# Kernel tuning notes

Hardware: AMD Instinct MI355X
Metric: run time of the kernel (lower is better)

Reference implementation:

```python
import jax, jax.numpy as jnp
import numpy as np

VOCAB, ENC, DEC, ATT, EMB = 10000, 2048, 512, 512, 512
B, P, L = 64, 196, 20


def setup_inputs() -> dict:
    key = jax.random.key(0)
    ks = jax.random.split(key, 24)
    s = lambda k, shape, fan: jax.random.normal(k, shape, jnp.float32) / np.sqrt(fan)
    inp = {
        "img_features": jax.random.normal(ks[0], (B, P, ENC), jnp.float32),
        "captions": jax.random.randint(ks[1], (B, L), 0, VOCAB),
        # init-state projections
        "W_init_h": s(ks[2], (DEC, ENC), ENC), "b_init_h": jnp.zeros((DEC,), jnp.float32),
        "W_init_c": s(ks[3], (DEC, ENC), ENC), "b_init_c": jnp.zeros((DEC,), jnp.float32),
        # attention
        "W_dec": s(ks[4], (ATT, DEC), DEC), "b_dec": jnp.zeros((ATT,), jnp.float32),
        "W_enc": s(ks[5], (ATT, ENC), ENC), "b_enc": jnp.zeros((ATT,), jnp.float32),
        "W_fin": s(ks[6], (1, ATT), ATT), "b_fin": jnp.zeros((1,), jnp.float32),
        # gate + output + embedding
        "W_gate": s(ks[7], (ENC, DEC), DEC), "b_gate": jnp.zeros((ENC,), jnp.float32),
        "W_out": s(ks[8], (VOCAB, DEC), DEC), "b_out": jnp.zeros((VOCAB,), jnp.float32),
        "emb": s(ks[9], (VOCAB, EMB), EMB),
        # LSTMCell (PyTorch gate order: i, f, g, o)
        "W_ih": s(ks[10], (4 * DEC, EMB + ENC), EMB + ENC), "b_ih": jnp.zeros((4 * DEC,), jnp.float32),
        "W_hh": s(ks[11], (4 * DEC, DEC), DEC), "b_hh": jnp.zeros((4 * DEC,), jnp.float32),
    }
    return inp


def _decode(img_features, captions, W_init_h, b_init_h, W_init_c, b_init_c,
            W_dec, b_dec, W_enc, b_enc, W_fin, b_fin,
            W_gate, b_gate, W_out, b_out, emb, W_ih, W_hh, b_ih, b_hh):
    # lengths are uniform (padded tensor), so sort/restore are identity and
    # batch_size_t == B at every step.
    avg = img_features.mean(axis=1)                              # [B,ENC]
    h0 = jnp.tanh(avg @ W_init_h.T + b_init_h)                   # [B,DEC]
    c0 = jnp.tanh(avg @ W_init_c.T + b_init_c)
    enc_proj = img_features @ W_enc.T + b_enc                    # [B,P,ATT] (loop-invariant)
    emb_seq = emb[captions[:, :-1]]                              # [B,T,EMB], T = L-1

    def step(carry, e_t):
        h, c = carry
        U_h = h @ W_dec.T + b_dec                                # [B,ATT]
        att = jnp.tanh(enc_proj + U_h[:, None, :])               # [B,P,ATT]
        e = (att @ W_fin.T + b_fin)[..., 0]                      # [B,P]
        alpha = jax.nn.softmax(e, axis=1)
        context = jnp.einsum('bpe,bp->be', img_features, alpha)  # [B,ENC]
        gate = jax.nn.sigmoid(h @ W_gate.T + b_gate)             # [B,ENC]
        x = jnp.concatenate([e_t, gate * context], axis=1)       # [B,EMB+ENC]
        gates = x @ W_ih.T + b_ih + h @ W_hh.T + b_hh            # [B,4*DEC]
        i, f, g, o = jnp.split(gates, 4, axis=1)
        c_new = jax.nn.sigmoid(f) * c + jax.nn.sigmoid(i) * jnp.tanh(g)
        h_new = jax.nn.sigmoid(o) * jnp.tanh(c_new)
        out = h_new @ W_out.T + b_out                            # [B,VOCAB] (dropout=eval identity)
        return (h_new, c_new), (out, alpha)

    _, (preds, alphas) = jax.lax.scan(step, (h0, c0), jnp.swapaxes(emb_seq, 0, 1))
    return jnp.swapaxes(preds, 0, 1), jnp.swapaxes(alphas, 0, 1)  # [B,T,VOCAB], [B,T,P]


def reference(img_features, captions, W_init_h, b_init_h, W_init_c, b_init_c,
              W_dec, b_dec, W_enc, b_enc, W_fin, b_fin,
              W_gate, b_gate, W_out, b_out, emb, W_ih, W_hh, b_ih, b_hh):
    return _decode(img_features, captions, W_init_h, b_init_h, W_init_c, b_init_c,
                   W_dec, b_dec, W_enc, b_enc, W_fin, b_fin,
                   W_gate, b_gate, W_out, b_out, emb, W_ih, W_hh, b_ih, b_hh)
```

## Files before the change

### kernel.cpp

```cpp
#include <hip/hip_runtime.h>
#include <hip/hip_bf16.h>

typedef unsigned short u16;
typedef unsigned int   u32;

#define BB    64
#define PP    196
#define ENC   2048
#define DEC   512
#define ATT   512
#define EMB   512
#define VOCAB 10000
#define VPAD2 10112
#define TT    19
#define LCAP  20
#define MALL  1280
#define XDIM  3072
#define LDSTR 40
#define LD64  72

typedef __bf16 bf16x8 __attribute__((ext_vector_type(8)));
typedef float  f32x4  __attribute__((ext_vector_type(4)));

__device__ __forceinline__ float bf2f(u16 u) {
  union { float f; u32 i; } v; v.i = ((u32)u) << 16; return v.f;
}
__device__ __forceinline__ u16 f2bf(float f) {
  u32 x = __float_as_uint(f);
  u32 r = (x + 0x7FFFu + ((x >> 16) & 1u)) >> 16;
  return (u16)r;
}
__device__ __forceinline__ u32 pack2(float a, float b) {
  return (u32)f2bf(a) | ((u32)f2bf(b) << 16);
}
__device__ __forceinline__ float wred_sum(float v) {
  #pragma unroll
  for (int off = 32; off > 0; off >>= 1) v += __shfl_xor(v, off, 64);
  return v;
}
__device__ __forceinline__ float wred_max(float v) {
  #pragma unroll
  for (int off = 32; off > 0; off >>= 1) v = fmaxf(v, __shfl_xor(v, off, 64));
  return v;
}
__device__ __forceinline__ float tanh_fast(float x) {
  return 1.f - 2.f / (__expf(2.f * x) + 1.f);
}
__device__ __forceinline__ float sigm(float x) {
  return 1.f / (1.f + __expf(-x));
}

__global__ __launch_bounds__(256) void k_cvt_simple(u16* __restrict__ dst,
    const float* __restrict__ src, int n4) {
  int stride = gridDim.x * blockDim.x;
  for (int i = blockIdx.x * blockDim.x + threadIdx.x; i < n4; i += stride) {
    float4 v = ((const float4*)src)[i];
    ((uint2*)dst)[i] = make_uint2(pack2(v.x, v.y), pack2(v.z, v.w));
  }
}

__global__ __launch_bounds__(256) void k_cvt_pad(u16* __restrict__ dst,
    const float* __restrict__ src) {
  int total = VPAD2 * (DEC / 2);
  int stride = gridDim.x * blockDim.x;
  for (int i = blockIdx.x * blockDim.x + threadIdx.x; i < total; i += stride) {
    int row = i >> 8, c2 = i & 255;
    u32 v = 0;
    if (row < VOCAB) {
      float2 f = ((const float2*)src)[(size_t)row * 256 + c2];
      v = pack2(f.x, f.y);
    }
    ((u32*)dst)[i] = v;
  }
}

__global__ __launch_bounds__(256) void k_cvt_comb(u16* __restrict__ dst,
    const float* __restrict__ Wih, const float* __restrict__ Whh) {
  int j = blockIdx.x;
  for (int t = threadIdx.x; t < 768; t += 256) {
    int col = t * 4;
    float4 v = (col < 2560)
        ? ((const float4*)(Wih + (size_t)j * 2560))[t]
        : ((const float4*)(Whh + (size_t)j * 512))[(col - 2560) >> 2];
    ((uint2*)(dst + (size_t)j * XDIM))[t] = make_uint2(pack2(v.x, v.y), pack2(v.z, v.w));
  }
}

__global__ __launch_bounds__(256) void k_avg(const float* __restrict__ img,
    u16* __restrict__ avgb) {
  int b = blockIdx.x;
  int col = blockIdx.y * 256 + threadIdx.x;
  const float* base = img + (size_t)b * PP * ENC + col;
  float s = 0.f;
  for (int p = 0; p < PP; ++p) s += base[(size_t)p * ENC];
  avgb[b * ENC + col] = f2bf(s * (1.f / PP));
}

__global__ __launch_bounds__(256) void k_init_mfma(const u16* __restrict__ avgb,
    const u16* __restrict__ Winitb, const float* __restrict__ bh,
    const float* __restrict__ bc, u16* __restrict__ h, float* __restrict__ c) {
  __shared__ __align__(16) u16 As[2 * 64 * LD64];
  __shared__ __align__(16) u16 Bs[2 * 64 * LD64];
  int n0 = blockIdx.x * 64;
  int tid = threadIdx.x, wv = tid >> 6, lane = tid & 63;
  int wm = wv >> 1, wn = wv & 1;
  int fr = lane & 15, kg = (lane >> 4) * 8, rq = lane >> 4;
  int r0 = tid >> 3, kc0 = (tid & 7) * 8;
  int r1 = (tid + 256) >> 3, kc1 = ((tid + 256) & 7) * 8;
  uint4 pa0 = *(const uint4*)&avgb[(size_t)r0 * ENC + kc0];
  uint4 pa1 = *(const uint4*)&avgb[(size_t)r1 * ENC + kc1];
  uint4 pb0 = *(const uint4*)&Winitb[(size_t)(n0 + r0) * ENC + kc0];
  uint4 pb1 = *(const uint4*)&Winitb[(size_t)(n0 + r1) * ENC + kc1];
  f32x4 acc[2][2] = {};
  const int NK = ENC / 64;
  for (int kt = 0; kt < NK; ++kt) {
    u16* as = As + (kt & 1) * (64 * LD64);
    u16* bs = Bs + (kt & 1) * (64 * LD64);
    *(uint4*)&as[r0 * LD64 + kc0] = pa0;
    *(uint4*)&as[r1 * LD64 + kc1] = pa1;
    *(uint4*)&bs[r0 * LD64 + kc0] = pb0;
    *(uint4*)&bs[r1 * LD64 + kc1] = pb1;
    __syncthreads();
    if (kt + 1 < NK) {
      int k0 = (kt + 1) * 64;
      pa0 = *(const uint4*)&avgb[(size_t)r0 * ENC + k0 + kc0];
      pa1 = *(const uint4*)&avgb[(size_t)r1 * ENC + k0 + kc1];
      pb0 = *(const uint4*)&Winitb[(size_t)(n0 + r0) * ENC + k0 + kc0];
      pb1 = *(const uint4*)&Winitb[(size_t)(n0 + r1) * ENC + k0 + kc1];
    }
    #pragma unroll
    for (int ks = 0; ks < 2; ++ks) {
      bf16x8 a0 = *(const bf16x8*)&as[(wm * 32 + fr) * LD64 + ks * 32 + kg];
      bf16x8 a1 = *(const bf16x8*)&as[(wm * 32 + 16 + fr) * LD64 + ks * 32 + kg];
      bf16x8 b0 = *(const bf16x8*)&bs[(wn * 32 + fr) * LD64 + ks * 32 + kg];
      bf16x8 b1 = *(const bf16x8*)&bs[(wn * 32 + 16 + fr) * LD64 + ks * 32 + kg];
      acc[0][0] = __builtin_amdgcn_mfma_f32_16x16x32_bf16(a0, b0, acc[0][0], 0, 0, 0);
      acc[0][1] = __builtin_amdgcn_mfma_f32_16x16x32_bf16(a0, b1, acc[0][1], 0, 0, 0);
      acc[1][0] = __builtin_amdgcn_mfma_f32_16x16x32_bf16(a1, b0, acc[1][0], 0, 0, 0);
      acc[1][1] = __builtin_amdgcn_mfma_f32_16x16x32_bf16(a1, b1, acc[1][1], 0, 0, 0);
    }
  }
  #pragma unroll
  for (int mi = 0; mi < 2; ++mi)
    for (int ni = 0; ni < 2; ++ni)
      #pragma unroll
      for (int r = 0; r < 4; ++r) {
        int m = wm * 32 + mi * 16 + rq * 4 + r;
        int n = n0 + wn * 32 + ni * 16 + fr;
        float v = acc[mi][ni][r];
        if (n < DEC) h[m * DEC + n] = f2bf(tanh_fast(v + bh[n]));
        else         c[m * DEC + (n - DEC)] = tanh_fast(v + bc[n - DEC]);
      }
}

template <int SRC>
__global__ __launch_bounds__(256) void k_encproj(
    const u16* __restrict__ Ab, const float* __restrict__ Af,
    const u16* __restrict__ Wb, const float* __restrict__ Wf,
    const float* __restrict__ benc, u16* __restrict__ epj) {
  __shared__ __align__(16) u16 As[128 * LDSTR];
  __shared__ __align__(16) u16 Bs[128 * LDSTR];
  int m0 = blockIdx.x * 128, n0 = blockIdx.y * 128;
  int tid = threadIdx.x, wv = tid >> 6, lane = tid & 63;
  int wm = wv >> 1, wn = wv & 1;
  int fr = lane & 15, kg = (lane >> 4) * 8, rq = lane >> 4;
  f32x4 acc[4][4] = {};
  for (int k0 = 0; k0 < ENC; k0 += 32) {
    __syncthreads();
    #pragma unroll
    for (int i = 0; i < 2; ++i) {
      int id = tid + i * 256;
      int r = id >> 2, kc = id & 3;
      if (SRC == 0) {
        *(uint4*)(&As[r * LDSTR + kc * 8]) = *(const uint4*)(&Ab[(size_t)(m0 + r) * ENC + k0 + kc * 8]);
        *(uint4*)(&Bs[r * LDSTR + kc * 8]) = *(const uint4*)(&Wb[(size_t)(n0 + r) * ENC + k0 + kc * 8]);
      } else {
        const float* asrc = &Af[(size_t)(m0 + r) * ENC + k0 + kc * 8];
        float4 f0 = ((const float4*)asrc)[0];
        float4 f1 = ((const float4*)asrc)[1];
        *(uint4*)(&As[r * LDSTR + kc * 8]) =
            make_uint4(pack2(f0.x, f0.y), pack2(f0.z, f0.w),
                       pack2(f1.x, f1.y), pack2(f1.z, f1.w));
        const float* bsrc = &Wf[(size_t)(n0 + r) * ENC + k0 + kc * 8];
        float4 g0 = ((const float4*)bsrc)[0];
        float4 g1 = ((const float4*)bsrc)[1];
        *(uint4*)(&Bs[r * LDSTR + kc * 8]) =
            make_uint4(pack2(g0.x, g0.y), pack2(g0.z, g0.w),
                       pack2(g1.x, g1.y), pack2(g1.z, g1.w));
      }
    }
    __syncthreads();
    bf16x8 af[4], bfr[4];
    #pragma unroll
    for (int i = 0; i < 4; ++i) {
      af[i]  = *(const bf16x8*)(&As[(wm * 64 + i * 16 + fr) * LDSTR + kg]);
      bfr[i] = *(const bf16x8*)(&Bs[(wn * 64 + i * 16 + fr) * LDSTR + kg]);
    }
    #pragma unroll
    for (int mi = 0; mi < 4; ++mi)
      #pragma unroll
      for (int ni = 0; ni < 4; ++ni)
        acc[mi][ni] = __builtin_amdgcn_mfma_f32_16x16x32_bf16(af[mi], bfr[ni], acc[mi][ni], 0, 0, 0);
  }
  #pragma unroll
  for (int mi = 0; mi < 4; ++mi)
    for (int ni = 0; ni < 4; ++ni)
      #pragma unroll
      for (int r = 0; r < 4; ++r) {
        int m = m0 + wm * 64 + mi * 16 + rq * 4 + r;
        int n = n0 + wn * 64 + ni * 16 + fr;
        epj[(size_t)m * ATT + n] = f2bf(acc[mi][ni][r] + benc[n]);
      }
}

__global__ __launch_bounds__(256) void k_logits(const u16* __restrict__ hall,
    const u16* __restrict__ Woutb2, const float* __restrict__ bout,
    float* __restrict__ preds) {
  __shared__ __align__(16) u16 As[128 * LDSTR];
  __shared__ __align__(16) u16 Bs[128 * LDSTR];
  int m0 = blockIdx.x * 128, n0 = blockIdx.y * 128;
  int tid = threadIdx.x, wv = tid >> 6, lane = tid & 63;
  int wm = wv >> 1, wn = wv & 1;
  int fr = lane & 15, kg = (lane >> 4) * 8, rq = lane >> 4;
  f32x4 acc[4][4] = {};
  for (int k0 = 0; k0 < DEC; k0 += 32) {
    __syncthreads();
    #pragma unroll
    for (int i = 0; i < 2; ++i) {
      int id = tid + i * 256;
      int r = id >> 2, kc = id & 3;
      *(uint4*)(&As[r * LDSTR + kc * 8]) = *(const uint4*)(&hall[(size_t)(m0 + r) * DEC + k0 + kc * 8]);
      *(uint4*)(&Bs[r * LDSTR + kc * 8]) = *(const uint4*)(&Woutb2[(size_t)(n0 + r) * DEC + k0 + kc * 8]);
    }
    __syncthreads();
    bf16x8 af[4], bfr[4];
    #pragma unroll
    for (int i = 0; i < 4; ++i) {
      af[i]  = *(const bf16x8*)(&As[(wm * 64 + i * 16 + fr) * LDSTR + kg]);
      bfr[i] = *(const bf16x8*)(&Bs[(wn * 64 + i * 16 + fr) * LDSTR + kg]);
    }
    #pragma unroll
    for (int mi = 0; mi < 4; ++mi)
      #pragma unroll
      for (int ni = 0; ni < 4; ++ni)
        acc[mi][ni] = __builtin_amdgcn_mfma_f32_16x16x32_bf16(af[mi], bfr[ni], acc[mi][ni], 0, 0, 0);
  }
  #pragma unroll
  for (int mi = 0; mi < 4; ++mi)
    for (int ni = 0; ni < 4; ++ni)
      #pragma unroll
      for (int r = 0; r < 4; ++r) {
        int m = m0 + wm * 64 + mi * 16 + rq * 4 + r;
        int n = n0 + wn * 64 + ni * 16 + fr;
        if (m < TT * BB && n < VOCAB) {
          int t = m >> 6, b = m & 63;
          preds[(size_t)b * (TT * VOCAB) + (size_t)t * VOCAB + n] = acc[mi][ni][r] + bout[n];
        }
      }
}

__global__ __launch_bounds__(256) void k_hcons(const u16* __restrict__ h,
    const u16* __restrict__ Wdecb, const float* __restrict__ bdec,
    const u16* __restrict__ Wgateb, const float* __restrict__ bgate,
    float* __restrict__ uh, float* __restrict__ gate, u16* __restrict__ x) {
  __shared__ __align__(16) u16 As[2 * 64 * LD64];
  __shared__ __align__(16) u16 Bs[2 * 64 * LD64];
  int bid = blockIdx.x;
  int tid = threadIdx.x, wv = tid >> 6, lane = tid & 63;
  int wm = wv >> 1, wn = wv & 1;
  int fr = lane & 15, kg = (lane >> 4) * 8, rq = lane >> 4;

  if (bid == 0) {
    for (int i = tid; i < 16384; i += 256) {
      int b = i >> 8, jp = (i & 255) * 2;
      *(u32*)(&x[(size_t)b * XDIM + 2560 + jp]) = *(const u32*)(&h[b * DEC + jp]);
    }
  }

  int role, nt; const u16* Wsrc;
  if (bid < 8) { role = 0; nt = bid;     Wsrc = Wdecb;  }
  else         { role = 1; nt = bid - 8; Wsrc = Wgateb; }
  int n0 = nt * 64;

  int r0 = tid >> 3, kc0 = (tid & 7) * 8;
  int r1 = (tid + 256) >> 3, kc1 = ((tid + 256) & 7) * 8;
  uint4 pa0 = *(const uint4*)&h[(size_t)r0 * DEC + kc0];
  uint4 pa1 = *(const uint4*)&h[(size_t)r1 * DEC + kc1];
  uint4 pb0 = *(const uint4*)&Wsrc[(size_t)(n0 + r0) * DEC + kc0];
  uint4 pb1 = *(const uint4*)&Wsrc[(size_t)(n0 + r1) * DEC + kc1];
  f32x4 acc[2][2] = {};
  const int NK = DEC / 64;
  for (int kt = 0; kt < NK; ++kt) {
    u16* as = As + (kt & 1) * (64 * LD64);
    u16* bs = Bs + (kt & 1) * (64 * LD64);
    *(uint4*)&as[r0 * LD64 + kc0] = pa0;
    *(uint4*)&as[r1 * LD64 + kc1] = pa1;
    *(uint4*)&bs[r0 * LD64 + kc0] = pb0;
    *(uint4*)&bs[r1 * LD64 + kc1] = pb1;
    __syncthreads();
    if (kt + 1 < NK) {
      int k0 = (kt + 1) * 64;
      pa0 = *(const uint4*)&h[(size_t)r0 * DEC + k0 + kc0];
      pa1 = *(const uint4*)&h[(size_t)r1 * DEC + k0 + kc1];
      pb0 = *(const uint4*)&Wsrc[(size_t)(n0 + r0) * DEC + k0 + kc0];
      pb1 = *(const uint4*)&Wsrc[(size_t)(n0 + r1) * DEC + k0 + kc1];
    }
    #pragma unroll
    for (int ks = 0; ks < 2; ++ks) {
      bf16x8 a0 = *(const bf16x8*)&as[(wm * 32 + fr) * LD64 + ks * 32 + kg];
      bf16x8 a1 = *(const bf16x8*)&as[(wm * 32 + 16 + fr) * LD64 + ks * 32 + kg];
      bf16x8 b0 = *(const bf16x8*)&bs[(wn * 32 + fr) * LD64 + ks * 32 + kg];
      bf16x8 b1 = *(const bf16x8*)&bs[(wn * 32 + 16 + fr) * LD64 + ks * 32 + kg];
      acc[0][0] = __builtin_amdgcn_mfma_f32_16x16x32_bf16(a0, b0, acc[0][0], 0, 0, 0);
      acc[0][1] = __builtin_amdgcn_mfma_f32_16x16x32_bf16(a0, b1, acc[0][1], 0, 0, 0);
      acc[1][0] = __builtin_amdgcn_mfma_f32_16x16x32_bf16(a1, b0, acc[1][0], 0, 0, 0);
      acc[1][1] = __builtin_amdgcn_mfma_f32_16x16x32_bf16(a1, b1, acc[1][1], 0, 0, 0);
    }
  }
  #pragma unroll
  for (int mi = 0; mi < 2; ++mi)
    for (int ni = 0; ni < 2; ++ni)
      #pragma unroll
      for (int r = 0; r < 4; ++r) {
        int m = wm * 32 + mi * 16 + rq * 4 + r;
        int n = n0 + wn * 32 + ni * 16 + fr;
        float v = acc[mi][ni][r];
        if (role == 0) uh[m * DEC + n] = v + bdec[n];
        else           gate[m * ENC + n] = sigm(v + bgate[n]);
      }
}

__global__ __launch_bounds__(256) void k_escore(const float* __restrict__ uh,
    const u16* __restrict__ epj, const float* __restrict__ wfin, const float* __restrict__ bfin,
    const int* __restrict__ captions, const float* __restrict__ emb,
    float* __restrict__ e_ws, u16* __restrict__ x, int step) {
  __shared__ float s_uh[ATT], s_wf[ATT];
  int b = blockIdx.x, pt = blockIdx.y;
  int tid = threadIdx.x;
  for (int i = tid; i < ATT; i += 256) { s_uh[i] = uh[b * ATT + i]; s_wf[i] = wfin[i]; }
  __syncthreads();
  if (pt == 0) {
    int capv = captions[b * LCAP + step];
    float2 f = ((const float2*)(emb + (size_t)capv * EMB))[tid];
    ((u32*)(x + (size_t)b * XDIM))[tid] = pack2(f.x, f.y);
  }
  int w = tid >> 6, lane = tid & 63;
  float b0 = bfin[0];
  for (int pl = w; pl < 49; pl += 4) {
    int p = pt * 49 + pl;
    const u16* row = epj + (size_t)(b * PP + p) * ATT;
    float acc = 0.f;
    #pragma unroll
    for (int ki = 0; ki < 8; ++ki) {
      int a = lane + ki * 64;
      acc += tanh_fast(bf2f(row[a]) + s_uh[a]) * s_wf[a];
    }
    acc = wred_sum(acc);
    if (lane == 0) e_ws[b * PP + p] = acc + b0;
  }
}

template <int SRC>
__global__ __launch_bounds__(256) void k_ctx(const float* __restrict__ e_ws,
    const float* __restrict__ gate, const u16* __restrict__ imgb,
    const float* __restrict__ imgf,
    u16* __restrict__ x, float* __restrict__ alphas, int step) {
  __shared__ float s_a[PP];
  int b = blockIdx.x, et = blockIdx.y;
  int tid = threadIdx.x;
  if (tid < PP) s_a[tid] = e_ws[b * PP + tid];
  __syncthreads();
  if (tid < 64) {
    float v0 = s_a[tid], v1 = s_a[tid + 64], v2 = s_a[tid + 128];
    float v3 = (tid + 192 < PP) ? s_a[tid + 192] : -1e30f;
    float m = wred_max(fmaxf(fmaxf(v0, v1), fmaxf(v2, v3)));
    float e0 = __expf(v0 - m), e1 = __expf(v1 - m), e2 = __expf(v2 - m);
    float e3 = (tid + 192 < PP) ? __expf(v3 - m) : 0.f;
    float inv = 1.f / wred_sum(e0 + e1 + e2 + e3);
    s_a[tid] = e0 * inv; s_a[tid + 64] = e1 * inv; s_a[tid + 128] = e2 * inv;
    if (tid + 192 < PP) s_a[tid + 192] = e3 * inv;
  }
  __syncthreads();
  if (et == 0 && tid < PP)
    alphas[(size_t)b * (TT * PP) + (size_t)step * PP + tid] = s_a[tid];
  int e0i = et * 512 + tid * 2;
  float c0 = 0.f, c1 = 0.f;
  if (SRC == 0) {
    const u16* ib = imgb + (size_t)b * PP * ENC + e0i;
    for (int p = 0; p < PP; ++p) {
      u32 v = *(const u32*)(ib + (size_t)p * ENC);
      float ap = s_a[p];
      c0 += ap * bf2f((u16)(v & 0xFFFF));
      c1 += ap * bf2f((u16)(v >> 16));
    }
  } else {
    const float* ib = imgf + (size_t)b * PP * ENC + e0i;
    for (int p = 0; p < PP; ++p) {
      float2 v = *(const float2*)(ib + (size_t)p * ENC);
      float ap = s_a[p];
      c0 += ap * v.x;
      c1 += ap * v.y;
    }
  }
  float g0 = gate[b * ENC + e0i], g1 = gate[b * ENC + e0i + 1];
  *(u32*)(&x[(size_t)b * XDIM + 512 + e0i]) = pack2(c0 * g0, c1 * g1);
}

__global__ __launch_bounds__(256) void k_lstm_part(const u16* __restrict__ x,
    const u16* __restrict__ Wcomb, float* __restrict__ pbuf) {
  __shared__ __align__(16) u16 As[2 * 64 * LD64];
  __shared__ __align__(16) u16 Bs[2 * 64 * LD64];
  int jt = blockIdx.x, ksp = blockIdx.y;
  int kbase = ksp * 768;
  int tid = threadIdx.x, wv = tid >> 6, lane = tid & 63;
  int wm = wv >> 1, wn = wv & 1;
  int fr = lane & 15, kg = (lane >> 4) * 8, rq = lane >> 4;
  int r0 = tid >> 3, kc0 = (tid & 7) * 8;
  int r1 = (tid + 256) >> 3, kc1 = ((tid + 256) & 7) * 8;
  int wrow0 = (r0 >> 4) * 512 + jt * 16 + (r0 & 15);
  int wrow1 = (r1 >> 4) * 512 + jt * 16 + (r1 & 15);
  uint4 pa0 = *(const uint4*)&x[(size_t)r0 * XDIM + kbase + kc0];
  uint4 pa1 = *(const uint4*)&x[(size_t)r1 * XDIM + kbase + kc1];
  uint4 pb0 = *(const uint4*)&Wcomb[(size_t)wrow0 * XDIM + kbase + kc0];
  uint4 pb1 = *(const uint4*)&Wcomb[(size_t)wrow1 * XDIM + kbase + kc1];
  f32x4 acc[2][2] = {};
  const int NK = 12;
  for (int kt = 0; kt < NK; ++kt) {
    u16* as = As + (kt & 1) * (64 * LD64);
    u16* bs = Bs + (kt & 1) * (64 * LD64);
    *(uint4*)&as[r0 * LD64 + kc0] = pa0;
    *(uint4*)&as[r1 * LD64 + kc1] = pa1;
    *(uint4*)&bs[r0 * LD64 + kc0] = pb0;
    *(uint4*)&bs[r1 * LD64 + kc1] = pb1;
    __syncthreads();
    if (kt + 1 < NK) {
      int k0 = kbase + (kt + 1) * 64;
      pa0 = *(const uint4*)&x[(size_t)r0 * XDIM + k0 + kc0];
      pa1 = *(const uint4*)&x[(size_t)r1 * XDIM + k0 + kc1];
      pb0 = *(const uint4*)&Wcomb[(size_t)wrow0 * XDIM + k0 + kc0];
      pb1 = *(const uint4*)&Wcomb[(size_t)wrow1 * XDIM + k0 + kc1];
    }
    #pragma unroll
    for (int ks = 0; ks < 2; ++ks) {
      bf16x8 a0 = *(const bf16x8*)&as[(wm * 32 + fr) * LD64 + ks * 32 + kg];
      bf16x8 a1 = *(const bf16x8*)&as[(wm * 32 + 16 + fr) * LD64 + ks * 32 + kg];
      bf16x8 b0 = *(const bf16x8*)&bs[(wn * 32 + fr) * LD64 + ks * 32 + kg];
      bf16x8 b1 = *(const bf16x8*)&bs[(wn * 32 + 16 + fr) * LD64 + ks * 32 + kg];
      acc[0][0] = __builtin_amdgcn_mfma_f32_16x16x32_bf16(a0, b0, acc[0][0], 0, 0, 0);
      acc[0][1] = __builtin_amdgcn_mfma_f32_16x16x32_bf16(a0, b1, acc[0][1], 0, 0, 0);
      acc[1][0] = __builtin_amdgcn_mfma_f32_16x16x32_bf16(a1, b0, acc[1][0], 0, 0, 0);
      acc[1][1] = __builtin_amdgcn_mfma_f32_16x16x32_bf16(a1, b1, acc[1][1], 0, 0, 0);
    }
  }
  float* pout = pbuf + (size_t)(ksp * 32 + jt) * 4096;
  #pragma unroll
  for (int mi = 0; mi < 2; ++mi)
    for (int ni = 0; ni < 2; ++ni)
      #pragma unroll
      for (int r = 0; r < 4; ++r) {
        int m = wm * 32 + mi * 16 + rq * 4 + r;
        int n = wn * 32 + ni * 16 + fr;
        pout[m * 64 + n] = acc[mi][ni][r];
      }
}

__global__ __launch_bounds__(256) void k_lstm_fin(const float* __restrict__ pbuf,
    const float* __restrict__ bih, const float* __restrict__ bhh,
    float* __restrict__ c, u16* __restrict__ h, u16* __restrict__ hall, int step) {
  int jt = blockIdx.x, tid = threadIdx.x;
  #pragma unroll
  for (int ii = 0; ii < 4; ++ii) {
    int idx = tid + ii * 256;
    int bb = idx >> 4, jj = idx & 15;
    int j = jt * 16 + jj;
    float g4[4];
    #pragma unroll
    for (int g = 0; g < 4; ++g) {
      float s = 0.f;
      #pragma unroll
      for (int ks = 0; ks < 4; ++ks)
        s += pbuf[(size_t)(ks * 32 + jt) * 4096 + bb * 64 + g * 16 + jj];
      g4[g] = s;
    }
    float iv = g4[0] + bih[j]        + bhh[j];
    float fv = g4[1] + bih[512 + j]  + bhh[512 + j];
    float gv = g4[2] + bih[1024 + j] + bhh[1024 + j];
    float ov = g4[3] + bih[1536 + j] + bhh[1536 + j];
    float co = c[bb * DEC + j];
    float cn = sigm(fv) * co + sigm(iv) * tanh_fast(gv);
    float hn = sigm(ov) * tanh_fast(cn);
    c[bb * DEC + j] = cn;
    u16 hb = f2bf(hn);
    h[bb * DEC + j] = hb;
    hall[(size_t)(step * BB + bb) * DEC + j] = hb;
  }
}

extern "C" void kernel_launch(void* const* d_in, const int* in_sizes, int n_in,
                              void* d_out, int out_size, void* d_ws, size_t ws_size,
                              hipStream_t stream) {
  const float* img   = (const float*)d_in[0];
  const int*   cap   = (const int*)  d_in[1];
  const float* Winh  = (const float*)d_in[2];
  const float* binh  = (const float*)d_in[3];
  const float* Winc  = (const float*)d_in[4];
  const float* binc  = (const float*)d_in[5];
  const float* Wdec  = (const float*)d_in[6];
  const float* bdec  = (const float*)d_in[7];
  const float* Wenc  = (const float*)d_in[8];
  const float* benc  = (const float*)d_in[9];
  const float* Wfin  = (const float*)d_in[10];
  const float* bfin  = (const float*)d_in[11];
  const float* Wgate = (const float*)d_in[12];
  const float* bgate = (const float*)d_in[13];
  const float* Wout  = (const float*)d_in[14];
  const float* bout  = (const float*)d_in[15];
  const float* emb   = (const float*)d_in[16];
  const float* Wih   = (const float*)d_in[17];
  const float* bih   = (const float*)d_in[18];
  const float* Whh   = (const float*)d_in[19];
  const float* bhh   = (const float*)d_in[20];

  char* ws = (char*)d_ws;
  u16*   epj    = (u16*)  (ws);
  u16*   Winitb = (u16*)  (ws);
  u16*   avgb   = (u16*)  (ws + 4194304);
  u16*   Wcomb  = (u16*)  (ws + 12845056);
  u16*   Woutb2 = (u16*)  (ws + 25427968);
  u16*   Wgateb = (u16*)  (ws + 35782656);
  u16*   Wdecb  = (u16*)  (ws + 37879808);
  u16*   Wencb  = (u16*)  (ws + 38404096);
  float* pbuf   = (float*)(ws + 40501248);
  u16*   h      = (u16*)  (ws + 42598400);
  float* c      = (float*)(ws + 42663936);
  float* e_ws   = (float*)(ws + 42795008);
  u16*   x      = (u16*)  (ws + 42846208);
  float* uh     = (float*)(ws + 43239424);
  float* gate   = (float*)(ws + 43370496);
  u16*   hall   = (u16*)  (ws + 43894784);
  u16*   imgb   = (u16*)  (ws + 45205504);
  const bool use_imgb = (ws_size >= 96585728ull);

  float* preds  = (float*)d_out;
  float* alphas = (float*)d_out + (size_t)BB * TT * VOCAB;

  k_cvt_simple<<<512,  256, 0, stream>>>(Winitb,             Winh, 262144);
  k_cvt_simple<<<512,  256, 0, stream>>>(Winitb + 512 * ENC, Winc, 262144);
  if (use_imgb) {
    k_cvt_simple<<<4096, 256, 0, stream>>>(imgb,  img,  6422528);
    k_cvt_simple<<<512,  256, 0, stream>>>(Wencb, Wenc, 262144);
  }
  k_cvt_simple<<<512,  256, 0, stream>>>(Wgateb, Wgate, 262144);
  k_cvt_simple<<<128,  256, 0, stream>>>(Wdecb,  Wdec,  65536);
  k_cvt_pad   <<<2048, 256, 0, stream>>>(Woutb2, Wout);
  k_cvt_comb  <<<2048, 256, 0, stream>>>(Wcomb,  Wih, Whh);

  k_avg<<<dim3(BB, 8), 256, 0, stream>>>(img, avgb);
  k_init_mfma<<<16, 256, 0, stream>>>(avgb, Winitb, binh, binc, h, c);
  if (use_imgb)
    k_encproj<0><<<dim3(98, 4), 256, 0, stream>>>(imgb, img, Wencb, Wenc, benc, epj);
  else
    k_encproj<1><<<dim3(98, 4), 256, 0, stream>>>(imgb, img, Wencb, Wenc, benc, epj);
  k_hcons<<<40, 256, 0, stream>>>(h, Wdecb, bdec, Wgateb, bgate, uh, gate, x);
  for (int t = 0; t < TT; ++t) {
    k_escore<<<dim3(BB, 4), 256, 0, stream>>>(uh, epj, Wfin, bfin, cap, emb, e_ws, x, t);
    if (use_imgb)
      k_ctx<0><<<dim3(BB, 4), 256, 0, stream>>>(e_ws, gate, imgb, img, x, alphas, t);
    else
      k_ctx<1><<<dim3(BB, 4), 256, 0, stream>>>(e_ws, gate, imgb, img, x, alphas, t);
    k_lstm_part<<<dim3(32, 4), 256, 0, stream>>>(x, Wcomb, pbuf);
    k_lstm_fin<<<32, 256, 0, stream>>>(pbuf, bih, bhh, c, h, hall, t);
    if (t + 1 < TT)
      k_hcons<<<40, 256, 0, stream>>>(h, Wdecb, bdec, Wgateb, bgate, uh, gate, x);
  }
  k_logits<<<dim3(10, 79), 256, 0, stream>>>(hall, Woutb2, bout, preds);
}
```

Measured before the change: 1.200 ms.

## Fuse decoder projection, attention scores and softmax into one per-step front kernel

Merges k_hcons and k_escore into a single k_front launch per step. 64 blocks, one per batch row, compute U_h with a per-row dot product against a transposed bf16 W_dec, then the attention scores and the softmax. The other 16 blocks compute the gate GEMM with 128-wide tiles. The softmax and the alphas write move out of k_ctx, so each k_ctx block no longer recomputes them. This removes one launch per step and the uh global round trip. In exchange, each of the 64 batch blocks redoes the full 512x512 W_dec matvec, and the attention pass runs with 64 blocks instead of 256.

```diff
diff --git a/kernel.cpp b/kernel.cpp
--- a/kernel.cpp
+++ b/kernel.cpp
@@ -14,7 +14,6 @@
 #define VPAD2 10112
 #define TT    19
 #define LCAP  20
-#define MALL  1280
 #define XDIM  3072
 #define LDSTR 40
 #define LD64  72
@@ -84,6 +83,17 @@
         : ((const float4*)(Whh + (size_t)j * 512))[(col - 2560) >> 2];
     ((uint2*)(dst + (size_t)j * XDIM))[t] = make_uint2(pack2(v.x, v.y), pack2(v.z, v.w));
   }
+}
+
+__global__ __launch_bounds__(256) void k_cvt_dect(u16* __restrict__ dst,
+    const float* __restrict__ Wdec) {
+  int idx = blockIdx.x * 256 + threadIdx.x;
+  int k0 = idx >> 9, j = idx & 511;
+  const float* src = Wdec + (size_t)j * DEC + k0 * 8;
+  float4 f0 = ((const float4*)src)[0];
+  float4 f1 = ((const float4*)src)[1];
+  ((uint4*)dst)[idx] = make_uint4(pack2(f0.x, f0.y), pack2(f0.z, f0.w),
+                                  pack2(f1.x, f1.y), pack2(f1.z, f1.w));
 }
 
 __global__ __launch_bounds__(256) void k_avg(const float* __restrict__ img,
@@ -259,95 +269,95 @@
       }
 }
 
-__global__ __launch_bounds__(256) void k_hcons(const u16* __restrict__ h,
-    const u16* __restrict__ Wdecb, const float* __restrict__ bdec,
+__global__ __launch_bounds__(512) void k_front(const u16* __restrict__ h,
+    const u16* __restrict__ WdecT2, const float* __restrict__ bdec,
     const u16* __restrict__ Wgateb, const float* __restrict__ bgate,
-    float* __restrict__ uh, float* __restrict__ gate, u16* __restrict__ x) {
-  __shared__ __align__(16) u16 As[2 * 64 * LD64];
-  __shared__ __align__(16) u16 Bs[2 * 64 * LD64];
+    const u16* __restrict__ epj, const float* __restrict__ wfin,
+    const float* __restrict__ bfin, const int* __restrict__ captions,
+    const float* __restrict__ emb,
+    float* __restrict__ gate, float* __restrict__ e_ws,
+    u16* __restrict__ x, float* __restrict__ alphas, int step) {
+  __shared__ __align__(16) u16 smem[2 * 64 * LD64 + 2 * 128 * LD64];
   int bid = blockIdx.x;
   int tid = threadIdx.x, wv = tid >> 6, lane = tid & 63;
-  int wm = wv >> 1, wn = wv & 1;
-  int fr = lane & 15, kg = (lane >> 4) * 8, rq = lane >> 4;
-
-  if (bid == 0) {
-    for (int i = tid; i < 16384; i += 256) {
-      int b = i >> 8, jp = (i & 255) * 2;
-      *(u32*)(&x[(size_t)b * XDIM + 2560 + jp]) = *(const u32*)(&h[b * DEC + jp]);
-    }
-  }
-
-  int role, nt; const u16* Wsrc;
-  if (bid < 8) { role = 0; nt = bid;     Wsrc = Wdecb;  }
-  else         { role = 1; nt = bid - 8; Wsrc = Wgateb; }
-  int n0 = nt * 64;
-
-  int r0 = tid >> 3, kc0 = (tid & 7) * 8;
-  int r1 = (tid + 256) >> 3, kc1 = ((tid + 256) & 7) * 8;
-  uint4 pa0 = *(const uint4*)&h[(size_t)r0 * DEC + kc0];
-  uint4 pa1 = *(const uint4*)&h[(size_t)r1 * DEC + kc1];
-  uint4 pb0 = *(const uint4*)&Wsrc[(size_t)(n0 + r0) * DEC + kc0];
-  uint4 pb1 = *(const uint4*)&Wsrc[(size_t)(n0 + r1) * DEC + kc1];
-  f32x4 acc[2][2] = {};
-  const int NK = DEC / 64;
-  for (int kt = 0; kt < NK; ++kt) {
-    u16* as = As + (kt & 1) * (64 * LD64);
-    u16* bs = Bs + (kt & 1) * (64 * LD64);
-    *(uint4*)&as[r0 * LD64 + kc0] = pa0;
-    *(uint4*)&as[r1 * LD64 + kc1] = pa1;
-    *(uint4*)&bs[r0 * LD64 + kc0] = pb0;
-    *(uint4*)&bs[r1 * LD64 + kc1] = pb1;
-    __syncthreads();
-    if (kt + 1 < NK) {
-      int k0 = (kt + 1) * 64;
-      pa0 = *(const uint4*)&h[(size_t)r0 * DEC + k0 + kc0];
-      pa1 = *(const uint4*)&h[(size_t)r1 * DEC + k0 + kc1];
-      pb0 = *(const uint4*)&Wsrc[(size_t)(n0 + r0) * DEC + k0 + kc0];
-      pb1 = *(const uint4*)&Wsrc[(size_t)(n0 + r1) * DEC + k0 + kc1];
-    }
-    #pragma unroll
-    for (int ks = 0; ks < 2; ++ks) {
-      bf16x8 a0 = *(const bf16x8*)&as[(wm * 32 + fr) * LD64 + ks * 32 + kg];
-      bf16x8 a1 = *(const bf16x8*)&as[(wm * 32 + 16 + fr) * LD64 + ks * 32 + kg];
-      bf16x8 b0 = *(const bf16x8*)&bs[(wn * 32 + fr) * LD64 + ks * 32 + kg];
-      bf16x8 b1 = *(const bf16x8*)&bs[(wn * 32 + 16 + fr) * LD64 + ks * 32 + kg];
-      acc[0][0] = __builtin_amdgcn_mfma_f32_16x16x32_bf16(a0, b0, acc[0][0], 0, 0, 0);
-      acc[0][1] = __builtin_amdgcn_mfma_f32_16x16x32_bf16(a0, b1, acc[0][1], 0, 0, 0);
-      acc[1][0] = __builtin_amdgcn_mfma_f32_16x16x32_bf16(a1, b0, acc[1][0], 0, 0, 0);
-      acc[1][1] = __builtin_amdgcn_mfma_f32_16x16x32_bf16(a1, b1, acc[1][1], 0, 0, 0);
-    }
-  }
-  #pragma unroll
-  for (int mi = 0; mi < 2; ++mi)
-    for (int ni = 0; ni < 2; ++ni)
-      #pragma unroll
-      for (int r = 0; r < 4; ++r) {
-        int m = wm * 32 + mi * 16 + rq * 4 + r;
-        int n = n0 + wn * 32 + ni * 16 + fr;
-        float v = acc[mi][ni][r];
-        if (role == 0) uh[m * DEC + n] = v + bdec[n];
-        else           gate[m * ENC + n] = sigm(v + bgate[n]);
-      }
-}
-
-__global__ __launch_bounds__(256) void k_escore(const float* __restrict__ uh,
-    const u16* __restrict__ epj, const float* __restrict__ wfin, const float* __restrict__ bfin,
-    const int* __restrict__ captions, const float* __restrict__ emb,
-    float* __restrict__ e_ws, u16* __restrict__ x, int step) {
-  __shared__ float s_uh[ATT], s_wf[ATT];
-  int b = blockIdx.x, pt = blockIdx.y;
-  int tid = threadIdx.x;
-  for (int i = tid; i < ATT; i += 256) { s_uh[i] = uh[b * ATT + i]; s_wf[i] = wfin[i]; }
-  __syncthreads();
-  if (pt == 0) {
+
+  if (bid >= 64) {
+    u16* As = smem;
+    u16* Bs = smem + 2 * 64 * LD64;
+    int n0 = (bid - 64) * 128;
+    int wm = wv >> 2, wn = wv & 3;
+    int fr = lane & 15, kgr = (lane >> 4) * 8, rq = lane >> 4;
+    int r0 = tid >> 3, kc0 = (tid & 7) * 8;
+    uint4 pa  = *(const uint4*)&h[(size_t)r0 * DEC + kc0];
+    uint4 pb0 = *(const uint4*)&Wgateb[(size_t)(n0 + r0) * DEC + kc0];
+    uint4 pb1 = *(const uint4*)&Wgateb[(size_t)(n0 + 64 + r0) * DEC + kc0];
+    f32x4 acc[2][2] = {};
+    const int NK = DEC / 64;
+    for (int kt = 0; kt < NK; ++kt) {
+      u16* as = As + (kt & 1) * (64 * LD64);
+      u16* bs = Bs + (kt & 1) * (128 * LD64);
+      *(uint4*)&as[r0 * LD64 + kc0] = pa;
+      *(uint4*)&bs[r0 * LD64 + kc0] = pb0;
+      *(uint4*)&bs[(64 + r0) * LD64 + kc0] = pb1;
+      __syncthreads();
+      if (kt + 1 < NK) {
+        int k0 = (kt + 1) * 64;
+        pa  = *(const uint4*)&h[(size_t)r0 * DEC + k0 + kc0];
+        pb0 = *(const uint4*)&Wgateb[(size_t)(n0 + r0) * DEC + k0 + kc0];
+        pb1 = *(const uint4*)&Wgateb[(size_t)(n0 + 64 + r0) * DEC + k0 + kc0];
+      }
+      #pragma unroll
+      for (int ks = 0; ks < 2; ++ks) {
+        bf16x8 a0 = *(const bf16x8*)&as[(wm * 32 + fr) * LD64 + ks * 32 + kgr];
+        bf16x8 a1 = *(const bf16x8*)&as[(wm * 32 + 16 + fr) * LD64 + ks * 32 + kgr];
+        bf16x8 b0 = *(const bf16x8*)&bs[(wn * 32 + fr) * LD64 + ks * 32 + kgr];
+        bf16x8 b1 = *(const bf16x8*)&bs[(wn * 32 + 16 + fr) * LD64 + ks * 32 + kgr];
+        acc[0][0] = __builtin_amdgcn_mfma_f32_16x16x32_bf16(a0, b0, acc[0][0], 0, 0, 0);
+        acc[0][1] = __builtin_amdgcn_mfma_f32_16x16x32_bf16(a0, b1, acc[0][1], 0, 0, 0);
+        acc[1][0] = __builtin_amdgcn_mfma_f32_16x16x32_bf16(a1, b0, acc[1][0], 0, 0, 0);
+        acc[1][1] = __builtin_amdgcn_mfma_f32_16x16x32_bf16(a1, b1, acc[1][1], 0, 0, 0);
+      }
+    }
+    #pragma unroll
+    for (int mi = 0; mi < 2; ++mi)
+      for (int ni = 0; ni < 2; ++ni)
+        #pragma unroll
+        for (int r = 0; r < 4; ++r) {
+          int m = wm * 32 + mi * 16 + rq * 4 + r;
+          int n = n0 + wn * 32 + ni * 16 + fr;
+          gate[m * ENC + n] = sigm(acc[mi][ni][r] + bgate[n]);
+        }
+    return;
+  }
+
+  float* s_h  = (float*)smem;
+  float* s_uh = s_h + DEC;
+  float* s_wf = s_uh + ATT;
+  float* s_e  = s_wf + ATT;
+  int b = bid;
+  s_h[tid] = bf2f(h[b * DEC + tid]);
+  s_wf[tid] = wfin[tid];
+  if (tid < 256) {
     int capv = captions[b * LCAP + step];
     float2 f = ((const float2*)(emb + (size_t)capv * EMB))[tid];
     ((u32*)(x + (size_t)b * XDIM))[tid] = pack2(f.x, f.y);
-  }
-  int w = tid >> 6, lane = tid & 63;
+    ((u32*)(x + (size_t)b * XDIM + 2560))[tid] = ((const u32*)(h + (size_t)b * DEC))[tid];
+  }
+  __syncthreads();
+  {
+    float acc = bdec[tid];
+    #pragma unroll 4
+    for (int k0 = 0; k0 < 64; ++k0) {
+      bf16x8 wrow = *(const bf16x8*)&WdecT2[(size_t)(k0 * 512 + tid) * 8];
+      #pragma unroll
+      for (int kk = 0; kk < 8; ++kk)
+        acc += s_h[k0 * 8 + kk] * (float)wrow[kk];
+    }
+    s_uh[tid] = acc;
+  }
+  __syncthreads();
   float b0 = bfin[0];
-  for (int pl = w; pl < 49; pl += 4) {
-    int p = pt * 49 + pl;
+  for (int p = wv; p < PP; p += 8) {
     const u16* row = epj + (size_t)(b * PP + p) * ATT;
     float acc = 0.f;
     #pragma unroll
@@ -356,33 +366,36 @@
       acc += tanh_fast(bf2f(row[a]) + s_uh[a]) * s_wf[a];
     }
     acc = wred_sum(acc);
-    if (lane == 0) e_ws[b * PP + p] = acc + b0;
+    if (lane == 0) s_e[p] = acc + b0;
+  }
+  __syncthreads();
+  if (tid < 64) {
+    float v0 = s_e[tid], v1 = s_e[tid + 64], v2 = s_e[tid + 128];
+    float v3 = (tid + 192 < PP) ? s_e[tid + 192] : -1e30f;
+    float m = wred_max(fmaxf(fmaxf(v0, v1), fmaxf(v2, v3)));
+    float e0 = __expf(v0 - m), e1 = __expf(v1 - m), e2 = __expf(v2 - m);
+    float e3 = (tid + 192 < PP) ? __expf(v3 - m) : 0.f;
+    float inv = 1.f / wred_sum(e0 + e1 + e2 + e3);
+    s_e[tid] = e0 * inv; s_e[tid + 64] = e1 * inv; s_e[tid + 128] = e2 * inv;
+    if (tid + 192 < PP) s_e[tid + 192] = e3 * inv;
+  }
+  __syncthreads();
+  if (tid < PP) {
+    float a = s_e[tid];
+    alphas[(size_t)b * (TT * PP) + (size_t)step * PP + tid] = a;
+    e_ws[b * PP + tid] = a;
   }
 }
 
 template <int SRC>
 __global__ __launch_bounds__(256) void k_ctx(const float* __restrict__ e_ws,
     const float* __restrict__ gate, const u16* __restrict__ imgb,
-    const float* __restrict__ imgf,
-    u16* __restrict__ x, float* __restrict__ alphas, int step) {
+    const float* __restrict__ imgf, u16* __restrict__ x) {
   __shared__ float s_a[PP];
   int b = blockIdx.x, et = blockIdx.y;
   int tid = threadIdx.x;
   if (tid < PP) s_a[tid] = e_ws[b * PP + tid];
   __syncthreads();
-  if (tid < 64) {
-    float v0 = s_a[tid], v1 = s_a[tid + 64], v2 = s_a[tid + 128];
-    float v3 = (tid + 192 < PP) ? s_a[tid + 192] : -1e30f;
-    float m = wred_max(fmaxf(fmaxf(v0, v1), fmaxf(v2, v3)));
-    float e0 = __expf(v0 - m), e1 = __expf(v1 - m), e2 = __expf(v2 - m);
-    float e3 = (tid + 192 < PP) ? __expf(v3 - m) : 0.f;
-    float inv = 1.f / wred_sum(e0 + e1 + e2 + e3);
-    s_a[tid] = e0 * inv; s_a[tid + 64] = e1 * inv; s_a[tid + 128] = e2 * inv;
-    if (tid + 192 < PP) s_a[tid + 192] = e3 * inv;
-  }
-  __syncthreads();
-  if (et == 0 && tid < PP)
-    alphas[(size_t)b * (TT * PP) + (size_t)step * PP + tid] = s_a[tid];
   int e0i = et * 512 + tid * 2;
   float c0 = 0.f, c1 = 0.f;
   if (SRC == 0) {
@@ -528,14 +541,13 @@
   u16*   Wcomb  = (u16*)  (ws + 12845056);
   u16*   Woutb2 = (u16*)  (ws + 25427968);
   u16*   Wgateb = (u16*)  (ws + 35782656);
-  u16*   Wdecb  = (u16*)  (ws + 37879808);
+  u16*   WdecT2 = (u16*)  (ws + 37879808);
   u16*   Wencb  = (u16*)  (ws + 38404096);
   float* pbuf   = (float*)(ws + 40501248);
   u16*   h      = (u16*)  (ws + 42598400);
   float* c      = (float*)(ws + 42663936);
   float* e_ws   = (float*)(ws + 42795008);
   u16*   x      = (u16*)  (ws + 42846208);
-  float* uh     = (float*)(ws + 43239424);
   float* gate   = (float*)(ws + 43370496);
   u16*   hall   = (u16*)  (ws + 43894784);
   u16*   imgb   = (u16*)  (ws + 45205504);
@@ -551,7 +563,7 @@
     k_cvt_simple<<<512,  256, 0, stream>>>(Wencb, Wenc, 262144);
   }
   k_cvt_simple<<<512,  256, 0, stream>>>(Wgateb, Wgate, 262144);
-  k_cvt_simple<<<128,  256, 0, stream>>>(Wdecb,  Wdec,  65536);
+  k_cvt_dect  <<<128,  256, 0, stream>>>(WdecT2, Wdec);
   k_cvt_pad   <<<2048, 256, 0, stream>>>(Woutb2, Wout);
   k_cvt_comb  <<<2048, 256, 0, stream>>>(Wcomb,  Wih, Whh);
 
@@ -561,17 +573,16 @@
     k_encproj<0><<<dim3(98, 4), 256, 0, stream>>>(imgb, img, Wencb, Wenc, benc, epj);
   else
     k_encproj<1><<<dim3(98, 4), 256, 0, stream>>>(imgb, img, Wencb, Wenc, benc, epj);
-  k_hcons<<<40, 256, 0, stream>>>(h, Wdecb, bdec, Wgateb, bgate, uh, gate, x);
+
   for (int t = 0; t < TT; ++t) {
-    k_escore<<<dim3(BB, 4), 256, 0, stream>>>(uh, epj, Wfin, bfin, cap, emb, e_ws, x, t);
+    k_front<<<80, 512, 0, stream>>>(h, WdecT2, bdec, Wgateb, bgate, epj, Wfin,
+                                    bfin, cap, emb, gate, e_ws, x, alphas, t);
     if (use_imgb)
-      k_ctx<0><<<dim3(BB, 4), 256, 0, stream>>>(e_ws, gate, imgb, img, x, alphas, t);
+      k_ctx<0><<<dim3(BB, 4), 256, 0, stream>>>(e_ws, gate, imgb, img, x);
     else
-      k_ctx<1><<<dim3(BB, 4), 256, 0, stream>>>(e_ws, gate, imgb, img, x, alphas, t);
+      k_ctx<1><<<dim3(BB, 4), 256, 0, stream>>>(e_ws, gate, imgb, img, x);
     k_lstm_part<<<dim3(32, 4), 256, 0, stream>>>(x, Wcomb, pbuf);
     k_lstm_fin<<<32, 256, 0, stream>>>(pbuf, bih, bhh, c, h, hall, t);
-    if (t + 1 < TT)
-      k_hcons<<<40, 256, 0, stream>>>(h, Wdecb, bdec, Wgateb, bgate, uh, gate, x);
   }
   k_logits<<<dim3(10, 79), 256, 0, stream>>>(hall, Woutb2, bout, preds);
 }
```

Result: slower. 1.234 ms (+2.9%).

## Fuse image bf16 conversion with mean pooling and deepen GEMM prefetch pipelines

Applied to the files above, without the earlier changes.

Merges the image fp32-to-bf16 conversion with the mean-over-pixels reduction so the 100MB image tensor is read once instead of twice. The encoder projection GEMM gains a double-buffered LDS with a two-stage register prefetch and a swizzled 1D block order that groups M tiles for L2 reuse of W_enc. The recurrent hcons and lstm_part kernels move from one-ahead to two-ahead register prefetch with fully unrolled loops. This costs extra registers and LDS, which may reduce occupancy.

```diff
diff --git a/kernel.cpp b/kernel.cpp
--- a/kernel.cpp
+++ b/kernel.cpp
@@ -14,7 +14,6 @@
 #define VPAD2 10112
 #define TT    19
 #define LCAP  20
-#define MALL  1280
 #define XDIM  3072
 #define LDSTR 40
 #define LD64  72
@@ -57,6 +56,20 @@
     float4 v = ((const float4*)src)[i];
     ((uint2*)dst)[i] = make_uint2(pack2(v.x, v.y), pack2(v.z, v.w));
   }
+}
+
+__global__ __launch_bounds__(256) void k_cvt_img(const float* __restrict__ img,
+    u16* __restrict__ imgb, u16* __restrict__ avgb) {
+  int b = blockIdx.x, col = blockIdx.y * 256 + threadIdx.x;
+  const float* base = img + (size_t)b * PP * ENC + col;
+  u16* obase = imgb + (size_t)b * PP * ENC + col;
+  float s = 0.f;
+  for (int p = 0; p < PP; ++p) {
+    float v = base[(size_t)p * ENC];
+    s += v;
+    obase[(size_t)p * ENC] = f2bf(v);
+  }
+  avgb[b * ENC + col] = f2bf(s * (1.f / PP));
 }
 
 __global__ __launch_bounds__(256) void k_cvt_pad(u16* __restrict__ dst,
@@ -86,11 +99,11 @@
   }
 }
 
-__global__ __launch_bounds__(256) void k_avg(const float* __restrict__ img,
+__global__ __launch_bounds__(256) void k_avg_f32(const float* __restrict__ imgf,
     u16* __restrict__ avgb) {
   int b = blockIdx.x;
   int col = blockIdx.y * 256 + threadIdx.x;
-  const float* base = img + (size_t)b * PP * ENC + col;
+  const float* base = imgf + (size_t)b * PP * ENC + col;
   float s = 0.f;
   for (int p = 0; p < PP; ++p) s += base[(size_t)p * ENC];
   avgb[b * ENC + col] = f2bf(s * (1.f / PP));
@@ -158,43 +171,65 @@
     const u16* __restrict__ Ab, const float* __restrict__ Af,
     const u16* __restrict__ Wb, const float* __restrict__ Wf,
     const float* __restrict__ benc, u16* __restrict__ epj) {
-  __shared__ __align__(16) u16 As[128 * LDSTR];
-  __shared__ __align__(16) u16 Bs[128 * LDSTR];
-  int m0 = blockIdx.x * 128, n0 = blockIdx.y * 128;
+  __shared__ __align__(16) u16 As[2 * 128 * LDSTR];
+  __shared__ __align__(16) u16 Bs[2 * 128 * LDSTR];
+  int bid = blockIdx.x;
+  int mt = (bid & 7) + 8 * (bid >> 5);
+  int nt = (bid >> 3) & 3;
+  if (mt >= 98) return;
+  int m0 = mt * 128, n0 = nt * 128;
   int tid = threadIdx.x, wv = tid >> 6, lane = tid & 63;
   int wm = wv >> 1, wn = wv & 1;
   int fr = lane & 15, kg = (lane >> 4) * 8, rq = lane >> 4;
+  int rr[2], kcc[2];
+  rr[0] = tid >> 2;          kcc[0] = (tid & 3) * 8;
+  rr[1] = (tid + 256) >> 2;  kcc[1] = ((tid + 256) & 3) * 8;
+
+  uint4 pA[2][2], pB[2][2];
+#define EP_LOAD(par, KT)                                                          \
+  {                                                                               \
+    int k0_ = (KT) * 32;                                                          \
+    _Pragma("unroll")                                                             \
+    for (int i_ = 0; i_ < 2; ++i_) {                                              \
+      if (SRC == 0) {                                                             \
+        pA[par][i_] = *(const uint4*)&Ab[(size_t)(m0 + rr[i_]) * ENC + k0_ + kcc[i_]]; \
+        pB[par][i_] = *(const uint4*)&Wb[(size_t)(n0 + rr[i_]) * ENC + k0_ + kcc[i_]]; \
+      } else {                                                                    \
+        const float* as_ = &Af[(size_t)(m0 + rr[i_]) * ENC + k0_ + kcc[i_]];      \
+        float4 f0_ = ((const float4*)as_)[0];                                     \
+        float4 f1_ = ((const float4*)as_)[1];                                     \
+        pA[par][i_] = make_uint4(pack2(f0_.x, f0_.y), pack2(f0_.z, f0_.w),        \
+                                 pack2(f1_.x, f1_.y), pack2(f1_.z, f1_.w));       \
+        const float* bs_ = &Wf[(size_t)(n0 + rr[i_]) * ENC + k0_ + kcc[i_]];      \
+        float4 g0_ = ((const float4*)bs_)[0];                                     \
+        float4 g1_ = ((const float4*)bs_)[1];                                     \
+        pB[par][i_] = make_uint4(pack2(g0_.x, g0_.y), pack2(g0_.z, g0_.w),        \
+                                 pack2(g1_.x, g1_.y), pack2(g1_.z, g1_.w));       \
+      }                                                                           \
+    }                                                                             \
+  }
+  EP_LOAD(0, 0);
+  EP_LOAD(1, 1);
   f32x4 acc[4][4] = {};
-  for (int k0 = 0; k0 < ENC; k0 += 32) {
-    __syncthreads();
+  #pragma unroll 4
+  for (int kt = 0; kt < 64; ++kt) {
+    u16* as = As + (kt & 1) * (128 * LDSTR);
+    u16* bs = Bs + (kt & 1) * (128 * LDSTR);
     #pragma unroll
     for (int i = 0; i < 2; ++i) {
-      int id = tid + i * 256;
-      int r = id >> 2, kc = id & 3;
-      if (SRC == 0) {
-        *(uint4*)(&As[r * LDSTR + kc * 8]) = *(const uint4*)(&Ab[(size_t)(m0 + r) * ENC + k0 + kc * 8]);
-        *(uint4*)(&Bs[r * LDSTR + kc * 8]) = *(const uint4*)(&Wb[(size_t)(n0 + r) * ENC + k0 + kc * 8]);
-      } else {
-        const float* asrc = &Af[(size_t)(m0 + r) * ENC + k0 + kc * 8];
-        float4 f0 = ((const float4*)asrc)[0];
-        float4 f1 = ((const float4*)asrc)[1];
-        *(uint4*)(&As[r * LDSTR + kc * 8]) =
-            make_uint4(pack2(f0.x, f0.y), pack2(f0.z, f0.w),
-                       pack2(f1.x, f1.y), pack2(f1.z, f1.w));
-        const float* bsrc = &Wf[(size_t)(n0 + r) * ENC + k0 + kc * 8];
-        float4 g0 = ((const float4*)bsrc)[0];
-        float4 g1 = ((const float4*)bsrc)[1];
-        *(uint4*)(&Bs[r * LDSTR + kc * 8]) =
-            make_uint4(pack2(g0.x, g0.y), pack2(g0.z, g0.w),
-                       pack2(g1.x, g1.y), pack2(g1.z, g1.w));
-      }
+      *(uint4*)&as[rr[i] * LDSTR + kcc[i]] = pA[kt & 1][i];
+      *(uint4*)&bs[rr[i] * LDSTR + kcc[i]] = pB[kt & 1][i];
+    }
+    if (kt + 2 < 64) {
+      int par = kt & 1;
+      EP_LOAD(par, kt + 2);
     }
     __syncthreads();
     bf16x8 af[4], bfr[4];
     #pragma unroll
     for (int i = 0; i < 4; ++i) {
-      af[i]  = *(const bf16x8*)(&As[(wm * 64 + i * 16 + fr) * LDSTR + kg]);
-      bfr[i] = *(const bf16x8*)(&Bs[(wn * 64 + i * 16 + fr) * LDSTR + kg]);
+      af[i]  = *(const bf16x8*)(&as[(wm * 64 + i * 16 + fr) * LDSTR + kg]);
+      bfr[i] = *(const bf16x8*)(&bs[(wn * 64 + i * 16 + fr) * LDSTR + kg]);
     }
     #pragma unroll
     for (int mi = 0; mi < 4; ++mi)
@@ -202,6 +237,7 @@
       for (int ni = 0; ni < 4; ++ni)
         acc[mi][ni] = __builtin_amdgcn_mfma_f32_16x16x32_bf16(af[mi], bfr[ni], acc[mi][ni], 0, 0, 0);
   }
+#undef EP_LOAD
   #pragma unroll
   for (int mi = 0; mi < 4; ++mi)
     for (int ni = 0; ni < 4; ++ni)
@@ -284,27 +320,29 @@
 
   int r0 = tid >> 3, kc0 = (tid & 7) * 8;
   int r1 = (tid + 256) >> 3, kc1 = ((tid + 256) & 7) * 8;
-  uint4 pa0 = *(const uint4*)&h[(size_t)r0 * DEC + kc0];
-  uint4 pa1 = *(const uint4*)&h[(size_t)r1 * DEC + kc1];
-  uint4 pb0 = *(const uint4*)&Wsrc[(size_t)(n0 + r0) * DEC + kc0];
-  uint4 pb1 = *(const uint4*)&Wsrc[(size_t)(n0 + r1) * DEC + kc1];
+  uint4 pa[2][2], pb[2][2];
+#define HC_LOAD(par, KT)                                                    \
+  {                                                                         \
+    int k0_ = (KT) * 64;                                                    \
+    pa[par][0] = *(const uint4*)&h[(size_t)r0 * DEC + k0_ + kc0];           \
+    pa[par][1] = *(const uint4*)&h[(size_t)r1 * DEC + k0_ + kc1];           \
+    pb[par][0] = *(const uint4*)&Wsrc[(size_t)(n0 + r0) * DEC + k0_ + kc0]; \
+    pb[par][1] = *(const uint4*)&Wsrc[(size_t)(n0 + r1) * DEC + k0_ + kc1]; \
+  }
+  HC_LOAD(0, 0);
+  HC_LOAD(1, 1);
   f32x4 acc[2][2] = {};
   const int NK = DEC / 64;
+  #pragma unroll
   for (int kt = 0; kt < NK; ++kt) {
     u16* as = As + (kt & 1) * (64 * LD64);
     u16* bs = Bs + (kt & 1) * (64 * LD64);
-    *(uint4*)&as[r0 * LD64 + kc0] = pa0;
-    *(uint4*)&as[r1 * LD64 + kc1] = pa1;
-    *(uint4*)&bs[r0 * LD64 + kc0] = pb0;
-    *(uint4*)&bs[r1 * LD64 + kc1] = pb1;
+    *(uint4*)&as[r0 * LD64 + kc0] = pa[kt & 1][0];
+    *(uint4*)&as[r1 * LD64 + kc1] = pa[kt & 1][1];
+    *(uint4*)&bs[r0 * LD64 + kc0] = pb[kt & 1][0];
+    *(uint4*)&bs[r1 * LD64 + kc1] = pb[kt & 1][1];
+    if (kt + 2 < NK) { HC_LOAD(kt & 1, kt + 2); }
     __syncthreads();
-    if (kt + 1 < NK) {
-      int k0 = (kt + 1) * 64;
-      pa0 = *(const uint4*)&h[(size_t)r0 * DEC + k0 + kc0];
-      pa1 = *(const uint4*)&h[(size_t)r1 * DEC + k0 + kc1];
-      pb0 = *(const uint4*)&Wsrc[(size_t)(n0 + r0) * DEC + k0 + kc0];
-      pb1 = *(const uint4*)&Wsrc[(size_t)(n0 + r1) * DEC + k0 + kc1];
-    }
     #pragma unroll
     for (int ks = 0; ks < 2; ++ks) {
       bf16x8 a0 = *(const bf16x8*)&as[(wm * 32 + fr) * LD64 + ks * 32 + kg];
@@ -317,6 +355,7 @@
       acc[1][1] = __builtin_amdgcn_mfma_f32_16x16x32_bf16(a1, b1, acc[1][1], 0, 0, 0);
     }
   }
+#undef HC_LOAD
   #pragma unroll
   for (int mi = 0; mi < 2; ++mi)
     for (int ni = 0; ni < 2; ++ni)
@@ -419,27 +458,29 @@
   int r1 = (tid + 256) >> 3, kc1 = ((tid + 256) & 7) * 8;
   int wrow0 = (r0 >> 4) * 512 + jt * 16 + (r0 & 15);
   int wrow1 = (r1 >> 4) * 512 + jt * 16 + (r1 & 15);
-  uint4 pa0 = *(const uint4*)&x[(size_t)r0 * XDIM + kbase + kc0];
-  uint4 pa1 = *(const uint4*)&x[(size_t)r1 * XDIM + kbase + kc1];
-  uint4 pb0 = *(const uint4*)&Wcomb[(size_t)wrow0 * XDIM + kbase + kc0];
-  uint4 pb1 = *(const uint4*)&Wcomb[(size_t)wrow1 * XDIM + kbase + kc1];
+  uint4 pa[2][2], pb[2][2];
+#define LP_LOAD(par, KT)                                                          \
+  {                                                                               \
+    int k0_ = kbase + (KT) * 64;                                                  \
+    pa[par][0] = *(const uint4*)&x[(size_t)r0 * XDIM + k0_ + kc0];                \
+    pa[par][1] = *(const uint4*)&x[(size_t)r1 * XDIM + k0_ + kc1];                \
+    pb[par][0] = *(const uint4*)&Wcomb[(size_t)wrow0 * XDIM + k0_ + kc0];         \
+    pb[par][1] = *(const uint4*)&Wcomb[(size_t)wrow1 * XDIM + k0_ + kc1];         \
+  }
+  LP_LOAD(0, 0);
+  LP_LOAD(1, 1);
   f32x4 acc[2][2] = {};
   const int NK = 12;
+  #pragma unroll
   for (int kt = 0; kt < NK; ++kt) {
     u16* as = As + (kt & 1) * (64 * LD64);
     u16* bs = Bs + (kt & 1) * (64 * LD64);
-    *(uint4*)&as[r0 * LD64 + kc0] = pa0;
-    *(uint4*)&as[r1 * LD64 + kc1] = pa1;
-    *(uint4*)&bs[r0 * LD64 + kc0] = pb0;
-    *(uint4*)&bs[r1 * LD64 + kc1] = pb1;
+    *(uint4*)&as[r0 * LD64 + kc0] = pa[kt & 1][0];
+    *(uint4*)&as[r1 * LD64 + kc1] = pa[kt & 1][1];
+    *(uint4*)&bs[r0 * LD64 + kc0] = pb[kt & 1][0];
+    *(uint4*)&bs[r1 * LD64 + kc1] = pb[kt & 1][1];
+    if (kt + 2 < NK) { LP_LOAD(kt & 1, kt + 2); }
     __syncthreads();
-    if (kt + 1 < NK) {
-      int k0 = kbase + (kt + 1) * 64;
-      pa0 = *(const uint4*)&x[(size_t)r0 * XDIM + k0 + kc0];
-      pa1 = *(const uint4*)&x[(size_t)r1 * XDIM + k0 + kc1];
-      pb0 = *(const uint4*)&Wcomb[(size_t)wrow0 * XDIM + k0 + kc0];
-      pb1 = *(const uint4*)&Wcomb[(size_t)wrow1 * XDIM + k0 + kc1];
-    }
     #pragma unroll
     for (int ks = 0; ks < 2; ++ks) {
       bf16x8 a0 = *(const bf16x8*)&as[(wm * 32 + fr) * LD64 + ks * 32 + kg];
@@ -452,6 +493,7 @@
       acc[1][1] = __builtin_amdgcn_mfma_f32_16x16x32_bf16(a1, b1, acc[1][1], 0, 0, 0);
     }
   }
+#undef LP_LOAD
   float* pout = pbuf + (size_t)(ksp * 32 + jt) * 4096;
   #pragma unroll
   for (int mi = 0; mi < 2; ++mi)
@@ -547,20 +589,21 @@
   k_cvt_simple<<<512,  256, 0, stream>>>(Winitb,             Winh, 262144);
   k_cvt_simple<<<512,  256, 0, stream>>>(Winitb + 512 * ENC, Winc, 262144);
   if (use_imgb) {
-    k_cvt_simple<<<4096, 256, 0, stream>>>(imgb,  img,  6422528);
-    k_cvt_simple<<<512,  256, 0, stream>>>(Wencb, Wenc, 262144);
+    k_cvt_img<<<dim3(BB, 8), 256, 0, stream>>>(img, imgb, avgb);
+    k_cvt_simple<<<512, 256, 0, stream>>>(Wencb, Wenc, 262144);
+  } else {
+    k_avg_f32<<<dim3(BB, 8), 256, 0, stream>>>(img, avgb);
   }
   k_cvt_simple<<<512,  256, 0, stream>>>(Wgateb, Wgate, 262144);
   k_cvt_simple<<<128,  256, 0, stream>>>(Wdecb,  Wdec,  65536);
   k_cvt_pad   <<<2048, 256, 0, stream>>>(Woutb2, Wout);
   k_cvt_comb  <<<2048, 256, 0, stream>>>(Wcomb,  Wih, Whh);
 
-  k_avg<<<dim3(BB, 8), 256, 0, stream>>>(img, avgb);
   k_init_mfma<<<16, 256, 0, stream>>>(avgb, Winitb, binh, binc, h, c);
   if (use_imgb)
-    k_encproj<0><<<dim3(98, 4), 256, 0, stream>>>(imgb, img, Wencb, Wenc, benc, epj);
+    k_encproj<0><<<416, 256, 0, stream>>>(imgb, img, Wencb, Wenc, benc, epj);
   else
-    k_encproj<1><<<dim3(98, 4), 256, 0, stream>>>(imgb, img, Wencb, Wenc, benc, epj);
+    k_encproj<1><<<416, 256, 0, stream>>>(imgb, img, Wencb, Wenc, benc, epj);
   k_hcons<<<40, 256, 0, stream>>>(h, Wdecb, bdec, Wgateb, bgate, uh, gate, x);
   for (int t = 0; t < TT; ++t) {
     k_escore<<<dim3(BB, 4), 256, 0, stream>>>(uh, epj, Wfin, bfin, cap, emb, e_ws, x, t);
```

After: 1.482 ms. +23.5%, slower.
